# Performance work log

Hardware: AMD Instinct MI355X
Metric: run time of the kernel (lower is better)

## Reference

```python
import jax, jax.numpy as jnp
import numpy as np

D = 768          # embedding_dim
H = 8            # attention heads
DH = D // H
HID = 512        # hidden_dim
N_LAYERS = 3     # graph conv layers
N_ETYPES = 5
LN_EPS = 1e-5


def setup_inputs() -> dict:
    key = jax.random.key(0)
    ks = jax.random.split(key, 32)
    N, E = 4096, 131072
    s = lambda fan: 1.0 / np.sqrt(fan)
    inp = {
        'node_features': jax.random.normal(ks[0], (N, D), jnp.float32),
        'edge_indices': jax.random.randint(ks[1], (2, E), 0, N, jnp.int64),
        'edge_types': jax.random.randint(ks[2], (E,), 0, N_ETYPES, jnp.int64),
        'node_types': jax.random.randint(ks[3], (N,), 0, 3, jnp.int64),
        # embedding tables
        'statute_emb': jax.random.normal(ks[4], (1000, D), jnp.float32),
        'case_emb': jax.random.normal(ks[5], (5000, D), jnp.float32),
        'article_emb': jax.random.normal(ks[6], (2000, D), jnp.float32),
        # per-layer conv params (stacked over 3 layers)
        'conv_msg_W': jax.random.uniform(ks[7], (N_LAYERS, N_ETYPES, D, D), jnp.float32, -s(D), s(D)),
        'conv_msg_b': jax.random.uniform(ks[8], (N_LAYERS, N_ETYPES, D), jnp.float32, -s(D), s(D)),
        'conv_upd_W': jax.random.uniform(ks[9], (N_LAYERS, D, 2 * D), jnp.float32, -s(2 * D), s(2 * D)),
        'conv_upd_b': jax.random.uniform(ks[10], (N_LAYERS, D), jnp.float32, -s(2 * D), s(2 * D)),
        'conv_ln_g': jnp.ones((N_LAYERS, D), jnp.float32),
        'conv_ln_b': jnp.zeros((N_LAYERS, D), jnp.float32),
        # MultiheadAttention params
        'in_proj_W': jax.random.uniform(ks[11], (3 * D, D), jnp.float32, -s(D), s(D)),
        'in_proj_b': jnp.zeros((3 * D,), jnp.float32),
        'out_proj_W': jax.random.uniform(ks[12], (D, D), jnp.float32, -s(D), s(D)),
        'out_proj_b': jnp.zeros((D,), jnp.float32),
        # network analyzer MLP
        'an_W1': jax.random.uniform(ks[13], (HID, D), jnp.float32, -s(D), s(D)),
        'an_b1': jax.random.uniform(ks[14], (HID,), jnp.float32, -s(D), s(D)),
        'an_W2': jax.random.uniform(ks[15], (HID // 2, HID), jnp.float32, -s(HID), s(HID)),
        'an_b2': jax.random.uniform(ks[16], (HID // 2,), jnp.float32, -s(HID), s(HID)),
        'an_W3': jax.random.uniform(ks[17], (1, HID // 2), jnp.float32, -s(HID // 2), s(HID // 2)),
        'an_b3': jax.random.uniform(ks[18], (1,), jnp.float32, -s(HID // 2), s(HID // 2)),
    }
    return inp


def _layer_norm(h, g, b):
    mu = h.mean(-1, keepdims=True)
    var = ((h - mu) ** 2).mean(-1, keepdims=True)
    return g * (h - mu) / jnp.sqrt(var + LN_EPS) + b


def _conv_layer(x, msg_W, msg_b, upd_W, upd_b, ln_g, ln_b, src, tgt, etypes):
    # x: [N, D]; src/tgt: [E]; etypes: [E]
    src_feats = x[src]                               # gather [E, D]
    agg = jnp.zeros_like(x)
    for t in range(N_ETYPES):                        # small fixed loop over edge types
        mask = (etypes == t)[:, None]
        msgs = jnp.where(mask, src_feats @ msg_W[t].T + msg_b[t], 0.0)
        agg = agg + jax.ops.segment_sum(msgs, tgt, num_segments=x.shape[0])
    combined = jnp.concatenate([x, agg], axis=-1)    # [N, 2D]
    upd = jax.nn.relu(combined @ upd_W.T + upd_b)    # dropout is identity in eval
    return _layer_norm(x + upd, ln_g, ln_b)


def reference(node_features, edge_indices, edge_types, node_types,
              statute_emb, case_emb, article_emb,
              conv_msg_W, conv_msg_b, conv_upd_W, conv_upd_b, conv_ln_g, conv_ln_b,
              in_proj_W, in_proj_b, out_proj_W, out_proj_b,
              an_W1, an_b1, an_W2, an_b2, an_W3, an_b3):
    N = node_features.shape[0]
    idx = jnp.arange(N)
    # per-node-type embedding lookup (i % table_size), vectorized
    emb = jnp.where((node_types == 0)[:, None], statute_emb[idx % 1000],
          jnp.where((node_types == 1)[:, None], case_emb[idx % 5000],
                    article_emb[idx % 2000]))
    x = node_features + emb

    src, tgt = edge_indices[0], edge_indices[1]
    for l in range(N_LAYERS):
        x = _conv_layer(x, conv_msg_W[l], conv_msg_b[l], conv_upd_W[l], conv_upd_b[l],
                        conv_ln_g[l], conv_ln_b[l], src, tgt, edge_types)

    # self-attention over all nodes (batch of 1), torch MHA semantics, eval mode
    qkv = x @ in_proj_W.T + in_proj_b                # [N, 3D]
    q, k, v = jnp.split(qkv, 3, axis=-1)
    to_h = lambda t: t.reshape(N, H, DH).transpose(1, 0, 2)   # [H, N, DH]
    q, k, v = to_h(q), to_h(k), to_h(v)
    scores = jnp.einsum('hqd,hkd->hqk', q, k) / jnp.sqrt(jnp.float32(DH))
    attn = jax.nn.softmax(scores, axis=-1)           # [H, N, N]
    ctx = jnp.einsum('hqk,hkd->hqd', attn, v).transpose(1, 0, 2).reshape(N, D)
    graph_repr = ctx @ out_proj_W.T + out_proj_b     # [N, D]
    attn_weights = attn.mean(0)                      # averaged over heads [N, N]

    pooled = graph_repr.mean(axis=0)                 # [D]
    h = jax.nn.relu(pooled @ an_W1.T + an_b1)
    h = jax.nn.relu(h @ an_W2.T + an_b2)
    network_score = jax.nn.sigmoid(h @ an_W3.T + an_b3)

    return x, graph_repr, network_score, attn_weights
```

## Files before the change

### kernel.cpp

```cpp
#include <hip/hip_runtime.h>

typedef unsigned short u16;
typedef unsigned int u32;
typedef __attribute__((ext_vector_type(4))) float f32x4;
typedef __attribute__((ext_vector_type(8))) __bf16 bf16x8;
typedef __attribute__((ext_vector_type(4))) unsigned int u32x4;
typedef __attribute__((ext_vector_type(2))) unsigned int u32x2;

#define DEV static __device__ __forceinline__

#define NNODE 4096
#define DMODEL 768
#define NEDGE 131072

static constexpr size_t OFF_X     = 0;
static constexpr size_t OFF_X2    = 12582912;
static constexpr size_t OFF_AMSG  = 25165824;
static constexpr size_t OFF_AUPD  = 31457280;
static constexpr size_t OFF_WMSG  = 44040192;
static constexpr size_t OFF_WUPD  = 61734912;
static constexpr size_t OFF_WIP   = 68812800;
static constexpr size_t OFF_WOP   = 72351744;
static constexpr size_t OFF_Q     = 73531392;
static constexpr size_t OFF_K     = 79822848;
static constexpr size_t OFF_V     = 86114304;
static constexpr size_t OFF_CTX   = 92405760;
static constexpr size_t OFF_STATS = 98697216;
static constexpr size_t OFF_ML    = 98959360;
static constexpr size_t OFF_DEG   = 100007936;
static constexpr size_t OFF_OFFS  = 100024320;
static constexpr size_t OFF_CUR   = 100040960;
static constexpr size_t OFF_PACK  = 100057344;
static constexpr size_t OFF_PART  = 100581632;
static constexpr size_t OFF_POOL  = 101368064;
static constexpr size_t OFF_H1    = 101371136;
static constexpr size_t OFF_H2    = 101373184;
static constexpr size_t OFF_Y     = 101374208;
static constexpr size_t WS_TOTAL  = 132831488;

__device__ __attribute__((aligned(256))) unsigned char g_ws[WS_TOTAL];

DEV u16 f2bf(float f) {
  return __builtin_bit_cast(u16, (__bf16)f);
}
DEV float bf2f(u16 h) {
  union { unsigned u; float f; } v; v.u = ((unsigned)h) << 16;
  return v.f;
}
DEV void gl_lds16(const void* g, void* l) {
  __builtin_amdgcn_global_load_lds((const __attribute__((address_space(1))) void*)g,
                                   (__attribute__((address_space(3))) void*)l, 16, 0, 0);
}
DEV f32x4 mfma16(bf16x8 a, bf16x8 b, f32x4 c) {
  return __builtin_amdgcn_mfma_f32_16x16x32_bf16(a, b, c, 0, 0, 0);
}
DEV void xcd_swz(int& z, int& bmy, int& bnx) {
  const int gx = gridDim.x, gy = gridDim.y;
  const int nwg = gx * gy * gridDim.z;
  const int L = blockIdx.x + gx * (blockIdx.y + gy * blockIdx.z);
  const int R = (L & 7) * (nwg >> 3) + (L >> 3);
  const int gxy = gx * gy;
  z = R / gxy;
  const int rem = R - z * gxy;
  bmy = rem / gx;
  bnx = rem - bmy * gx;
}

__global__ void zero_kernel(int* p, int n) {
  int i = blockIdx.x * 256 + threadIdx.x;
  if (i < n) p[i] = 0;
}
__global__ void deg_kernel(const int* __restrict__ ei, int* __restrict__ deg) {
  int e = blockIdx.x * 256 + threadIdx.x;
  atomicAdd(&deg[ei[NEDGE + e]], 1);
}
__global__ void scan_kernel(const int* __restrict__ deg, int* __restrict__ offs, int* __restrict__ cur) {
  __shared__ int buf[1024];
  int t = threadIdx.x;
  int v0 = deg[t*4], v1 = deg[t*4+1], v2 = deg[t*4+2], v3 = deg[t*4+3];
  int s = v0 + v1 + v2 + v3;
  buf[t] = s;
  __syncthreads();
  for (int off = 1; off < 1024; off <<= 1) {
    int add = (t >= off) ? buf[t - off] : 0;
    __syncthreads();
    buf[t] += add;
    __syncthreads();
  }
  int run = buf[t] - s;
  offs[t*4] = run; cur[t*4] = run; run += v0;
  offs[t*4+1] = run; cur[t*4+1] = run; run += v1;
  offs[t*4+2] = run; cur[t*4+2] = run; run += v2;
  offs[t*4+3] = run; cur[t*4+3] = run; run += v3;
  if (t == 1023) offs[4096] = run;
}
__global__ void scatter_kernel(const int* __restrict__ ei, const int* __restrict__ ety,
                               int* __restrict__ cur, int* __restrict__ pack) {
  int e = blockIdx.x * 256 + threadIdx.x;
  int tg = ei[NEDGE + e];
  int pos = atomicAdd(&cur[tg], 1);
  pack[pos] = ei[e] | (ety[e] << 12);
}

__global__ void convert_bf_kernel(const float* __restrict__ W, u16* __restrict__ out, int total4) {
  for (int i = blockIdx.x * 256 + threadIdx.x; i < total4; i += gridDim.x * 256) {
    f32x4 w = *(const f32x4*)(W + (size_t)i * 4);
    u32x2 o;
    o.x = (u32)f2bf(w.x) | ((u32)f2bf(w.y) << 16);
    o.y = (u32)f2bf(w.z) | ((u32)f2bf(w.w) << 16);
    *(u32x2*)(out + (size_t)i * 4) = o;
  }
}

__global__ void embed_kernel(const float* __restrict__ nf, const int* __restrict__ nty,
                             const float* __restrict__ se, const float* __restrict__ ce,
                             const float* __restrict__ ae,
                             float* __restrict__ x, u16* __restrict__ Amsg, u16* __restrict__ Aupd) {
  int v = blockIdx.x, t = threadIdx.x;
  int typ = nty[v];
  const float* tab = (typ == 0) ? se + (size_t)(v % 1000) * 768
                   : (typ == 1) ? ce + (size_t)(v % 5000) * 768
                                : ae + (size_t)(v % 2000) * 768;
  #pragma unroll
  for (int i = 0; i < 3; ++i) {
    int c = t + i * 256;
    float f = nf[(size_t)v * 768 + c] + tab[c];
    x[(size_t)v * 768 + c] = f;
    u16 hi = f2bf(f);
    Amsg[(size_t)v * 768 + c] = hi;
    Aupd[(size_t)v * 1536 + c] = hi;
  }
}

template<int EPI>
__global__ void __launch_bounds__(256, 3)
gemm_bt(const u16* __restrict__ A, int lda,
        const u16* __restrict__ B0, int ldb, int K,
        const float* __restrict__ bias0,
        float* __restrict__ C0, int ldc,
        const float* __restrict__ resid,
        u16* __restrict__ oq, u16* __restrict__ okk, u16* __restrict__ ov,
        long zsB, int zsBias, long zsC)
{
  __shared__ alignas(16) u16 sA[8192];
  __shared__ alignas(16) u16 sB[8192];
  const int tid = threadIdx.x;
  const int lane = tid & 63, wid = tid >> 6;
  const int wr = wid >> 1, wc = wid & 1;
  const int li = lane & 15, g = lane >> 4;
  int z, bmy, bnx;
  xcd_swz(z, bmy, bnx);
  const int bm = bmy * 128, bn = bnx * 128;
  const u16* B = B0 + (size_t)z * zsB;
  const float* bias = bias0 + (size_t)z * zsBias;

  const int srow = tid >> 3;
  const int scol = ((tid & 7) ^ (srow & 7)) * 8;
  const u16* Ag = A + (size_t)(bm + srow) * lda + scol;
  const u16* Bg = B + (size_t)(bn + srow) * ldb + scol;
  char* sAw = (char*)sA + wid * 1024;
  char* sBw = (char*)sB + wid * 1024;

  f32x4 acc[4][4];
  const f32x4 vz = {0.f, 0.f, 0.f, 0.f};
  #pragma unroll
  for (int i = 0; i < 4; ++i)
    #pragma unroll
    for (int j = 0; j < 4; ++j) acc[i][j] = vz;

  for (int k0 = 0; k0 < K; k0 += 64) {
    __syncthreads();
    #pragma unroll
    for (int is = 0; is < 4; ++is) {
      gl_lds16(Ag + (size_t)is * 32 * lda + k0, sAw + is * 4096);
      gl_lds16(Bg + (size_t)is * 32 * ldb + k0, sBw + is * 4096);
    }
    __syncthreads();
    #pragma unroll
    for (int kc = 0; kc < 2; ++kc) {
      bf16x8 av[4], bv[4];
      #pragma unroll
      for (int mt = 0; mt < 4; ++mt) {
        int row = wr * 64 + mt * 16 + li;
        av[mt] = *(const bf16x8*)((const char*)sA + row * 128 + ((kc * 64 + g * 16) ^ ((row & 7) << 4)));
      }
      #pragma unroll
      for (int nt = 0; nt < 4; ++nt) {
        int row = wc * 64 + nt * 16 + li;
        bv[nt] = *(const bf16x8*)((const char*)sB + row * 128 + ((kc * 64 + g * 16) ^ ((row & 7) << 4)));
      }
      #pragma unroll
      for (int mt = 0; mt < 4; ++mt)
        #pragma unroll
        for (int nt = 0; nt < 4; ++nt)
          acc[mt][nt] = mfma16(av[mt], bv[nt], acc[mt][nt]);
    }
  }
  #pragma unroll
  for (int mt = 0; mt < 4; ++mt) {
    #pragma unroll
    for (int nt = 0; nt < 4; ++nt) {
      #pragma unroll
      for (int r = 0; r < 4; ++r) {
        int gr = bm + wr * 64 + mt * 16 + g * 4 + r;
        int gc = bn + wc * 64 + nt * 16 + li;
        float v = acc[mt][nt][r] + bias[gc];
        if (EPI == 0) {
          C0[(size_t)z * zsC + (size_t)gr * ldc + gc] = v;
        } else if (EPI == 1) {
          C0[(size_t)gr * ldc + gc] = fmaxf(v, 0.f) + resid[(size_t)gr * 768 + gc];
        } else if (EPI == 3) {
          oq[(size_t)z * zsC + (size_t)gr * ldc + gc] = f2bf(v);
        } else {
          int part = gc / 768;
          int j = gc - part * 768;
          int h = j / 96, d = j - h * 96;
          if (part == 0)      oq[((size_t)(h << 12) + gr) * 96 + d] = f2bf(v * 0.10206207261596575f);
          else if (part == 1) okk[((size_t)(h << 12) + gr) * 96 + d] = f2bf(v);
          else                ov[((size_t)h * 96 + d) * 4096 + gr] = f2bf(v);
        }
      }
    }
  }
}

template<int EPI>
__global__ void __launch_bounds__(256, 3)
gemm_bt64(const u16* __restrict__ A, int lda,
          const u16* __restrict__ B0, int ldb, int K,
          const float* __restrict__ bias,
          float* __restrict__ C0, int ldc,
          const float* __restrict__ resid)
{
  __shared__ alignas(16) u16 sA[8192];
  __shared__ alignas(16) u16 sB[4096];
  const int tid = threadIdx.x;
  const int lane = tid & 63, wid = tid >> 6;
  const int wr = wid >> 1, wc = wid & 1;
  const int li = lane & 15, g = lane >> 4;
  int z, bmy, bnx;
  xcd_swz(z, bmy, bnx);
  const int bm = bmy * 128, bn = bnx * 64;

  const int srow = tid >> 3;
  const int scol = ((tid & 7) ^ (srow & 7)) * 8;
  const u16* Ag = A + (size_t)(bm + srow) * lda + scol;
  const u16* Bg = B0 + (size_t)(bn + srow) * ldb + scol;
  char* sAw = (char*)sA + wid * 1024;
  char* sBw = (char*)sB + wid * 1024;

  f32x4 acc[4][2];
  const f32x4 vz = {0.f, 0.f, 0.f, 0.f};
  #pragma unroll
  for (int i = 0; i < 4; ++i) { acc[i][0] = vz; acc[i][1] = vz; }

  for (int k0 = 0; k0 < K; k0 += 64) {
    __syncthreads();
    #pragma unroll
    for (int is = 0; is < 4; ++is)
      gl_lds16(Ag + (size_t)is * 32 * lda + k0, sAw + is * 4096);
    #pragma unroll
    for (int is = 0; is < 2; ++is)
      gl_lds16(Bg + (size_t)is * 32 * ldb + k0, sBw + is * 4096);
    __syncthreads();
    #pragma unroll
    for (int kc = 0; kc < 2; ++kc) {
      bf16x8 av[4], bv[2];
      #pragma unroll
      for (int mt = 0; mt < 4; ++mt) {
        int row = wr * 64 + mt * 16 + li;
        av[mt] = *(const bf16x8*)((const char*)sA + row * 128 + ((kc * 64 + g * 16) ^ ((row & 7) << 4)));
      }
      #pragma unroll
      for (int nt = 0; nt < 2; ++nt) {
        int row = wc * 32 + nt * 16 + li;
        bv[nt] = *(const bf16x8*)((const char*)sB + row * 128 + ((kc * 64 + g * 16) ^ ((row & 7) << 4)));
      }
      #pragma unroll
      for (int mt = 0; mt < 4; ++mt)
        #pragma unroll
        for (int nt = 0; nt < 2; ++nt)
          acc[mt][nt] = mfma16(av[mt], bv[nt], acc[mt][nt]);
    }
  }
  #pragma unroll
  for (int mt = 0; mt < 4; ++mt) {
    #pragma unroll
    for (int nt = 0; nt < 2; ++nt) {
      #pragma unroll
      for (int r = 0; r < 4; ++r) {
        int gr = bm + wr * 64 + mt * 16 + g * 4 + r;
        int gc = bn + wc * 32 + nt * 16 + li;
        float v = acc[mt][nt][r] + bias[gc];
        if (EPI == 0) C0[(size_t)gr * ldc + gc] = v;
        else          C0[(size_t)gr * ldc + gc] = fmaxf(v, 0.f) + resid[(size_t)gr * 768 + gc];
      }
    }
  }
}

__global__ void agg_kernel(const u16* __restrict__ Y, const int* __restrict__ offs,
                           const int* __restrict__ pack, u16* __restrict__ Aupd) {
  const int v = blockIdx.x, t = threadIdx.x;
  float a0 = 0.f, a1 = 0.f, a2 = 0.f, a3 = 0.f;
  const int beg = offs[v], end = offs[v + 1];
  const u32* Yw = (const u32*)Y;
  for (int i = beg; i < end; ++i) {
    int p = pack[i];
    u32x2 w = *(const u32x2*)(Yw + (size_t)p * 384 + t * 2);
    a0 += bf2f((u16)(w.x & 0xffffu));
    a1 += bf2f((u16)(w.x >> 16));
    a2 += bf2f((u16)(w.y & 0xffffu));
    a3 += bf2f((u16)(w.y >> 16));
  }
  u32x2 o;
  o.x = (u32)f2bf(a0) | ((u32)f2bf(a1) << 16);
  o.y = (u32)f2bf(a2) | ((u32)f2bf(a3) << 16);
  *(u32x2*)((u32*)(Aupd + (size_t)v * 1536 + 768) + t * 2) = o;
}

__global__ void ln_kernel(const float* __restrict__ xin, const float* __restrict__ gam,
                          const float* __restrict__ bet,
                          float* __restrict__ x, u16* __restrict__ Amsg, u16* __restrict__ Aupd,
                          float* __restrict__ xcopy) {
  __shared__ float red[256];
  int v = blockIdx.x, t = threadIdx.x;
  const float* r = xin + (size_t)v * 768;
  float v0 = r[t], v1 = r[t + 256], v2 = r[t + 512];
  red[t] = v0 + v1 + v2;
  __syncthreads();
  for (int off = 128; off > 0; off >>= 1) { if (t < off) red[t] += red[t + off]; __syncthreads(); }
  float mu = red[0] * (1.f / 768.f);
  __syncthreads();
  float d0 = v0 - mu, d1 = v1 - mu, d2 = v2 - mu;
  red[t] = d0 * d0 + d1 * d1 + d2 * d2;
  __syncthreads();
  for (int off = 128; off > 0; off >>= 1) { if (t < off) red[t] += red[t + off]; __syncthreads(); }
  float rstd = rsqrtf(red[0] * (1.f / 768.f) + 1e-5f);
  float dv[3] = {d0, d1, d2};
  #pragma unroll
  for (int i = 0; i < 3; ++i) {
    int c = t + i * 256;
    float y = gam[c] * dv[i] * rstd + bet[c];
    x[(size_t)v * 768 + c] = y;
    if (xcopy) xcopy[(size_t)v * 768 + c] = y;
    u16 hi = f2bf(y);
    Amsg[(size_t)v * 768 + c] = hi;
    Aupd[(size_t)v * 1536 + c] = hi;
  }
}

__global__ void __launch_bounds__(256, 3)
flash_kernel(const u16* __restrict__ Qb, const u16* __restrict__ Kb,
             const u16* __restrict__ Vtb, u16* __restrict__ Opb,
             float* __restrict__ Mp, float* __restrict__ Lp) {
  __shared__ alignas(16) u16 sK[6144];
  __shared__ alignas(16) u16 sV[6144];
  __shared__ alignas(16) u16 sP[4][2048];
  const int tid = threadIdx.x, lane = tid & 63, wid = tid >> 6;
  const int li = lane & 15, g = lane >> 4;
  const int R = blockIdx.x + 32 * (blockIdx.y + 8 * blockIdx.z);
  const int L = (R & 7) * 128 + (R >> 3);
  const int qt = L & 31, h = (L >> 5) & 7, kcb = L >> 8;
  const int vrow = tid >> 3, vcol = (tid & 7) ^ (vrow & 7);

  const u16* Qg = Qb + ((size_t)(h << 12) + qt * 128 + wid * 32 + li) * 96 + g * 8;
  bf16x8 aq0[3], aq1[3];
  #pragma unroll
  for (int kc = 0; kc < 3; ++kc) {
    aq0[kc] = *(const bf16x8*)(Qg + kc * 32);
    aq1[kc] = *(const bf16x8*)(Qg + 1536 + kc * 32);
  }

  float m0 = -1e30f, l0 = 0.f, m1 = -1e30f, l1 = 0.f;
  const f32x4 vz = {0.f, 0.f, 0.f, 0.f};
  f32x4 o0[6], o1[6];
  #pragma unroll
  for (int dt = 0; dt < 6; ++dt) { o0[dt] = vz; o1[dt] = vz; }

  const char* Kg = (const char*)(Kb + (size_t)(h << 12) * 96);
  const char* Vg = (const char*)(Vtb + (size_t)h * 96 * 4096);
  char* sKb = (char*)sK; char* sVb = (char*)sV; char* sPb = (char*)sP[wid];

  for (int kt = kcb * 16; kt < kcb * 16 + 16; ++kt) {
    __syncthreads();
    #pragma unroll
    for (int j = 0; j < 3; ++j) {
      gl_lds16(Kg + ((size_t)(kt * 64 + lane) * 96 + j * 32 + wid * 8) * 2, sKb + j * 4096 + wid * 1024);
      gl_lds16(Vg + (size_t)(j * 32 + vrow) * 8192 + kt * 128 + vcol * 16, sVb + j * 4096 + wid * 1024);
    }
    __syncthreads();

    f32x4 s0[4], s1[4];
    __builtin_amdgcn_s_setprio(1);
    #pragma unroll
    for (int nt = 0; nt < 4; ++nt) {
      s0[nt] = vz; s1[nt] = vz;
      #pragma unroll
      for (int kc = 0; kc < 3; ++kc) {
        bf16x8 bk = *(const bf16x8*)(sKb + kc * 4096 + g * 1024 + (nt * 16 + li) * 16);
        s0[nt] = mfma16(bk, aq0[kc], s0[nt]);
        s1[nt] = mfma16(bk, aq1[kc], s1[nt]);
      }
    }
    __builtin_amdgcn_s_setprio(0);

    {
      float mx = fmaxf(fmaxf(fmaxf(s0[0][0], s0[0][1]), fmaxf(s0[0][2], s0[0][3])),
                       fmaxf(fmaxf(s0[1][0], s0[1][1]), fmaxf(s0[1][2], s0[1][3])));
      mx = fmaxf(mx, fmaxf(fmaxf(fmaxf(s0[2][0], s0[2][1]), fmaxf(s0[2][2], s0[2][3])),
                           fmaxf(fmaxf(s0[3][0], s0[3][1]), fmaxf(s0[3][2], s0[3][3]))));
      mx = fmaxf(mx, __shfl_xor(mx, 16));
      mx = fmaxf(mx, __shfl_xor(mx, 32));
      float mnew = fmaxf(m0, mx);
      float alpha = __expf(m0 - mnew);
      float rs = 0.f;
      #pragma unroll
      for (int nt = 0; nt < 4; ++nt)
        #pragma unroll
        for (int r = 0; r < 4; ++r) { float p = __expf(s0[nt][r] - mnew); s0[nt][r] = p; rs += p; }
      rs += __shfl_xor(rs, 16);
      rs += __shfl_xor(rs, 32);
      l0 = l0 * alpha + rs;
      m0 = mnew;
      #pragma unroll
      for (int dt = 0; dt < 6; ++dt) o0[dt] *= alpha;
      #pragma unroll
      for (int nt = 0; nt < 4; ++nt)
        #pragma unroll
        for (int r0 = 0; r0 < 4; r0 += 2) {
          u32 w = (u32)f2bf(s0[nt][r0]) | ((u32)f2bf(s0[nt][r0 + 1]) << 16);
          *(u32*)(sPb + li * 128 + (((nt * 16 + g * 4 + r0) * 2) ^ ((li & 7) << 4))) = w;
        }
    }
    {
      float mx = fmaxf(fmaxf(fmaxf(s1[0][0], s1[0][1]), fmaxf(s1[0][2], s1[0][3])),
                       fmaxf(fmaxf(s1[1][0], s1[1][1]), fmaxf(s1[1][2], s1[1][3])));
      mx = fmaxf(mx, fmaxf(fmaxf(fmaxf(s1[2][0], s1[2][1]), fmaxf(s1[2][2], s1[2][3])),
                           fmaxf(fmaxf(s1[3][0], s1[3][1]), fmaxf(s1[3][2], s1[3][3]))));
      mx = fmaxf(mx, __shfl_xor(mx, 16));
      mx = fmaxf(mx, __shfl_xor(mx, 32));
      float mnew = fmaxf(m1, mx);
      float alpha = __expf(m1 - mnew);
      float rs = 0.f;
      #pragma unroll
      for (int nt = 0; nt < 4; ++nt)
        #pragma unroll
        for (int r = 0; r < 4; ++r) { float p = __expf(s1[nt][r] - mnew); s1[nt][r] = p; rs += p; }
      rs += __shfl_xor(rs, 16);
      rs += __shfl_xor(rs, 32);
      l1 = l1 * alpha + rs;
      m1 = mnew;
      #pragma unroll
      for (int dt = 0; dt < 6; ++dt) o1[dt] *= alpha;
      #pragma unroll
      for (int nt = 0; nt < 4; ++nt)
        #pragma unroll
        for (int r0 = 0; r0 < 4; r0 += 2) {
          u32 w = (u32)f2bf(s1[nt][r0]) | ((u32)f2bf(s1[nt][r0 + 1]) << 16);
          *(u32*)(sPb + (16 + li) * 128 + (((nt * 16 + g * 4 + r0) * 2) ^ ((li & 7) << 4))) = w;
        }
    }

    __builtin_amdgcn_s_setprio(1);
    #pragma unroll
    for (int kc2 = 0; kc2 < 2; ++kc2) {
      bf16x8 pa0 = *(const bf16x8*)(sPb + li * 128 + ((kc2 * 64 + g * 16) ^ ((li & 7) << 4)));
      bf16x8 pa1 = *(const bf16x8*)(sPb + (16 + li) * 128 + ((kc2 * 64 + g * 16) ^ ((li & 7) << 4)));
      #pragma unroll
      for (int dt = 0; dt < 6; ++dt) {
        int d = dt * 16 + li;
        bf16x8 bvv = *(const bf16x8*)(sVb + d * 128 + ((kc2 * 64 + g * 16) ^ ((d & 7) << 4)));
        o0[dt] = mfma16(pa0, bvv, o0[dt]);
        o1[dt] = mfma16(pa1, bvv, o1[dt]);
      }
    }
    __builtin_amdgcn_s_setprio(0);
  }
  int bq = qt * 128 + wid * 32;
  size_t cb = (size_t)(((kcb * 8 + h) << 12));
  #pragma unroll
  for (int dt = 0; dt < 6; ++dt)
    #pragma unroll
    for (int r = 0; r < 4; ++r) {
      int d = dt * 16 + li;
      Opb[(cb + bq + g * 4 + r) * 96 + d] = f2bf(o0[dt][r]);
      Opb[(cb + bq + 16 + g * 4 + r) * 96 + d] = f2bf(o1[dt][r]);
    }
  if (g == 0) {
    Mp[cb + bq + li] = m0;      Lp[cb + bq + li] = l0;
    Mp[cb + bq + 16 + li] = m1; Lp[cb + bq + 16 + li] = l1;
  }
}

__global__ void merge_kernel(const u16* __restrict__ Opb, const float* __restrict__ Mp,
                             const float* __restrict__ Lp,
                             u16* __restrict__ ctxb, float* __restrict__ stats) {
  int row = blockIdx.x, t = threadIdx.x;
  #pragma unroll
  for (int i = 0; i < 3; ++i) {
    int idx = t + i * 256;
    int h = idx / 96, d = idx - h * 96;
    int base = (h << 12) + row;
    float m0 = Mp[base], m1 = Mp[32768 + base], m2 = Mp[65536 + base], m3 = Mp[98304 + base];
    float M = fmaxf(fmaxf(m0, m1), fmaxf(m2, m3));
    float w0 = __expf(m0 - M), w1 = __expf(m1 - M), w2 = __expf(m2 - M), w3 = __expf(m3 - M);
    float L = w0 * Lp[base] + w1 * Lp[32768 + base] + w2 * Lp[65536 + base] + w3 * Lp[98304 + base];
    float o = w0 * bf2f(Opb[(size_t)base * 96 + d])
            + w1 * bf2f(Opb[(size_t)(32768 + base) * 96 + d])
            + w2 * bf2f(Opb[(size_t)(65536 + base) * 96 + d])
            + w3 * bf2f(Opb[(size_t)(98304 + base) * 96 + d]);
    float invl = 1.f / L;
    ctxb[(size_t)row * 768 + idx] = f2bf(o * invl);
    if (d == 0) {
      stats[base] = M;
      stats[32768 + base] = invl;
    }
  }
}

__global__ void __launch_bounds__(256, 3)
mean_kernel(const u16* __restrict__ Qb, const u16* __restrict__ Kb,
            const float* __restrict__ stats, float* __restrict__ out) {
  __shared__ alignas(16) u16 sQ[12288];
  __shared__ alignas(16) u16 sK2[6144];
  const int tid = threadIdx.x, lane = tid & 63, wid = tid >> 6;
  const int li = lane & 15, g = lane >> 4;
  const int q0 = blockIdx.x * 128, k0 = blockIdx.y * 64;
  const f32x4 vz = {0.f, 0.f, 0.f, 0.f};
  f32x4 macc0[4], macc1[4];
  #pragma unroll
  for (int nt = 0; nt < 4; ++nt) { macc0[nt] = vz; macc1[nt] = vz; }
  char* sQb = (char*)sQ; char* sKb = (char*)sK2;
  const int rq = (wid & 1) * 64 + lane;
  const int ccb = wid >> 1;

  for (int h = 0; h < 8; ++h) {
    __syncthreads();
    #pragma unroll
    for (int i = 0; i < 6; ++i) {
      int cc = i * 2 + ccb, kc = cc >> 2, gg = cc & 3;
      gl_lds16((const char*)Qb + ((size_t)(h << 12) + q0 + rq) * 192 + kc * 64 + gg * 16,
               sQb + kc * 8192 + gg * 2048 + (wid & 1) * 1024);
    }
    #pragma unroll
    for (int i = 0; i < 3; ++i) {
      int c = i * 4 + wid, kc = c >> 2, gg = c & 3;
      gl_lds16((const char*)Kb + ((size_t)(h << 12) + k0 + lane) * 192 + kc * 64 + gg * 16,
               sKb + kc * 4096 + gg * 1024);
    }
    __syncthreads();

    bf16x8 a20[3], a21[3];
    #pragma unroll
    for (int kc = 0; kc < 3; ++kc) {
      a20[kc] = *(const bf16x8*)(sQb + kc * 8192 + g * 2048 + (wid * 32 + li) * 16);
      a21[kc] = *(const bf16x8*)(sQb + kc * 8192 + g * 2048 + (wid * 32 + 16 + li) * 16);
    }
    f32x4 s0[4], s1[4];
    __builtin_amdgcn_s_setprio(1);
    #pragma unroll
    for (int nt = 0; nt < 4; ++nt) {
      s0[nt] = vz; s1[nt] = vz;
      #pragma unroll
      for (int kc = 0; kc < 3; ++kc) {
        bf16x8 bk = *(const bf16x8*)(sKb + kc * 4096 + g * 1024 + (nt * 16 + li) * 16);
        s0[nt] = mfma16(a20[kc], bk, s0[nt]);
        s1[nt] = mfma16(a21[kc], bk, s1[nt]);
      }
    }
    __builtin_amdgcn_s_setprio(0);
    #pragma unroll
    for (int r = 0; r < 4; ++r) {
      int row0 = q0 + wid * 32 + g * 4 + r;
      float mm0 = stats[(h << 12) + row0];
      float si0 = 0.125f * stats[32768 + (h << 12) + row0];
      int row1 = row0 + 16;
      float mm1 = stats[(h << 12) + row1];
      float si1 = 0.125f * stats[32768 + (h << 12) + row1];
      #pragma unroll
      for (int nt = 0; nt < 4; ++nt) {
        macc0[nt][r] += __expf(s0[nt][r] - mm0) * si0;
        macc1[nt][r] += __expf(s1[nt][r] - mm1) * si1;
      }
    }
  }
  #pragma unroll
  for (int nt = 0; nt < 4; ++nt)
    #pragma unroll
    for (int r = 0; r < 4; ++r) {
      out[(size_t)(q0 + wid * 32 + g * 4 + r) * 4096 + k0 + nt * 16 + li] = macc0[nt][r];
      out[(size_t)(q0 + wid * 32 + 16 + g * 4 + r) * 4096 + k0 + nt * 16 + li] = macc1[nt][r];
    }
}

__global__ void colsum_kernel(const float* __restrict__ gr, float* __restrict__ part) {
  int b = blockIdx.x, t = threadIdx.x;
  float s0 = 0.f, s1 = 0.f, s2 = 0.f;
  for (int rr = 0; rr < 16; ++rr) {
    const float* row = gr + (size_t)(b * 16 + rr) * 768;
    s0 += row[t]; s1 += row[t + 256]; s2 += row[t + 512];
  }
  part[b * 768 + t] = s0; part[b * 768 + t + 256] = s1; part[b * 768 + t + 512] = s2;
}
__global__ void pool_kernel(const float* __restrict__ part, float* __restrict__ pool) {
  int t = blockIdx.x * 256 + threadIdx.x;
  float s = 0.f;
  for (int b = 0; b < 256; ++b) s += part[b * 768 + t];
  pool[t] = s * (1.f / 4096.f);
}
template<int KDIM>
__global__ void mlp_fc_kernel(const float* __restrict__ in, const float* __restrict__ Wm,
                              const float* __restrict__ bb, float* __restrict__ outv) {
  int o = blockIdx.x * 4 + (threadIdx.x >> 6);
  int lane = threadIdx.x & 63;
  const float* w = Wm + (size_t)o * KDIM;
  float s = 0.f;
  #pragma unroll
  for (int k = lane; k < KDIM; k += 64) s += w[k] * in[k];
  s += __shfl_xor(s, 1);  s += __shfl_xor(s, 2);  s += __shfl_xor(s, 4);
  s += __shfl_xor(s, 8);  s += __shfl_xor(s, 16); s += __shfl_xor(s, 32);
  if (lane == 0) outv[o] = fmaxf(s + bb[o], 0.f);
}
__global__ void mlp3_kernel(const float* __restrict__ h2,
                            const float* __restrict__ W3, const float* __restrict__ b3,
                            float* __restrict__ out) {
  __shared__ float red[256];
  int t = threadIdx.x;
  red[t] = W3[t] * h2[t];
  __syncthreads();
  for (int off = 128; off > 0; off >>= 1) { if (t < off) red[t] += red[t + off]; __syncthreads(); }
  if (t == 0) out[0] = 1.f / (1.f + __expf(-(red[0] + b3[0])));
}

extern "C" void kernel_launch(void* const* d_in, const int* in_sizes, int n_in,
                              void* d_out, int out_size, void* d_ws, size_t ws_size,
                              hipStream_t stream) {
  const float* nf   = (const float*)d_in[0];
  const int*   ei   = (const int*)d_in[1];
  const int*   ety  = (const int*)d_in[2];
  const int*   nty  = (const int*)d_in[3];
  const float* se   = (const float*)d_in[4];
  const float* ce   = (const float*)d_in[5];
  const float* ae   = (const float*)d_in[6];
  const float* msgW = (const float*)d_in[7];
  const float* msgb = (const float*)d_in[8];
  const float* updW = (const float*)d_in[9];
  const float* updb = (const float*)d_in[10];
  const float* lng  = (const float*)d_in[11];
  const float* lnb  = (const float*)d_in[12];
  const float* ipW  = (const float*)d_in[13];
  const float* ipb  = (const float*)d_in[14];
  const float* opW  = (const float*)d_in[15];
  const float* opb  = (const float*)d_in[16];
  const float* aW1  = (const float*)d_in[17];
  const float* ab1  = (const float*)d_in[18];
  const float* aW2  = (const float*)d_in[19];
  const float* ab2  = (const float*)d_in[20];
  const float* aW3  = (const float*)d_in[21];
  const float* ab3  = (const float*)d_in[22];

  void* wsp = nullptr;
  hipGetSymbolAddress(&wsp, HIP_SYMBOL(g_ws));
  unsigned char* W = (unsigned char*)wsp;

  float* x     = (float*)(W + OFF_X);
  float* x2    = (float*)(W + OFF_X2);
  u16* Amsg    = (u16*)(W + OFF_AMSG);
  u16* Aupd    = (u16*)(W + OFF_AUPD);
  u16* Wmsg    = (u16*)(W + OFF_WMSG);
  u16* Wupd    = (u16*)(W + OFF_WUPD);
  u16* Wip     = (u16*)(W + OFF_WIP);
  u16* Wop     = (u16*)(W + OFF_WOP);
  u16* Qb      = (u16*)(W + OFF_Q);
  u16* Kb      = (u16*)(W + OFF_K);
  u16* Vtb     = (u16*)(W + OFF_V);
  u16* Ctxb    = (u16*)(W + OFF_CTX);
  float* stats = (float*)(W + OFF_STATS);
  float* Mp    = (float*)(W + OFF_ML);
  float* Lp    = Mp + 131072;
  int* deg     = (int*)(W + OFF_DEG);
  int* offs    = (int*)(W + OFF_OFFS);
  int* cur     = (int*)(W + OFF_CUR);
  int* pack    = (int*)(W + OFF_PACK);
  float* part  = (float*)(W + OFF_PART);
  float* pool  = (float*)(W + OFF_POOL);
  float* h1b   = (float*)(W + OFF_H1);
  float* h2b   = (float*)(W + OFF_H2);
  u16*   Yb    = (u16*)(W + OFF_Y);

  float* out_x    = (float*)d_out;
  float* out_gr   = out_x + (size_t)NNODE * DMODEL;
  float* out_sc   = out_gr + (size_t)NNODE * DMODEL;
  float* out_attn = out_sc + 1;
  u16*   Opb      = (u16*)out_attn;

  zero_kernel<<<16, 256, 0, stream>>>(deg, NNODE);
  deg_kernel<<<NEDGE / 256, 256, 0, stream>>>(ei, deg);
  scan_kernel<<<1, 1024, 0, stream>>>(deg, offs, cur);
  scatter_kernel<<<NEDGE / 256, 256, 0, stream>>>(ei, ety, cur, pack);

  convert_bf_kernel<<<2048, 256, 0, stream>>>(msgW, Wmsg, 3 * 5 * 768 * 768 / 4);
  convert_bf_kernel<<<1024, 256, 0, stream>>>(updW, Wupd, 3 * 768 * 1536 / 4);
  convert_bf_kernel<<<1024, 256, 0, stream>>>(ipW, Wip, 2304 * 768 / 4);
  convert_bf_kernel<<<512, 256, 0, stream>>>(opW, Wop, 768 * 768 / 4);

  embed_kernel<<<NNODE, 256, 0, stream>>>(nf, nty, se, ce, ae, x, Amsg, Aupd);

  for (int l = 0; l < 3; ++l) {
    gemm_bt<3><<<dim3(6, 32, 5), 256, 0, stream>>>(Amsg, 768,
        Wmsg + (size_t)l * 5 * 768 * 768, 768, 768,
        msgb + (size_t)l * 5 * 768, nullptr, 768, nullptr, Yb, nullptr, nullptr,
        (long)768 * 768, 768, (long)NNODE * DMODEL);
    agg_kernel<<<NNODE, 192, 0, stream>>>(Yb, offs, pack, Aupd);
    gemm_bt64<1><<<dim3(12, 32), 256, 0, stream>>>(Aupd, 1536,
        Wupd + (size_t)l * 768 * 1536, 1536, 1536,
        updb + (size_t)l * 768, x2, 768, x);
    ln_kernel<<<NNODE, 256, 0, stream>>>(x2, lng + (size_t)l * 768, lnb + (size_t)l * 768,
        x, Amsg, Aupd, (l == 2) ? out_x : nullptr);
  }

  gemm_bt<2><<<dim3(18, 32, 1), 256, 0, stream>>>(Amsg, 768, Wip, 768, 768,
      ipb, nullptr, 0, nullptr, Qb, Kb, Vtb, 0, 0, 0);
  flash_kernel<<<dim3(32, 8, 4), 256, 0, stream>>>(Qb, Kb, Vtb, Opb, Mp, Lp);
  merge_kernel<<<NNODE, 256, 0, stream>>>(Opb, Mp, Lp, Ctxb, stats);
  mean_kernel<<<dim3(32, 64), 256, 0, stream>>>(Qb, Kb, stats, out_attn);
  gemm_bt64<0><<<dim3(12, 32), 256, 0, stream>>>(Ctxb, 768, Wop, 768, 768,
      opb, out_gr, 768, nullptr);

  colsum_kernel<<<256, 256, 0, stream>>>(out_gr, part);
  pool_kernel<<<3, 256, 0, stream>>>(part, pool);
  mlp_fc_kernel<768><<<128, 256, 0, stream>>>(pool, aW1, ab1, h1b);
  mlp_fc_kernel<512><<<64, 256, 0, stream>>>(h1b, aW2, ab2, h2b);
  mlp3_kernel<<<1, 256, 0, stream>>>(h2b, aW3, ab3, out_sc);
}
```

Before: 607.2 us.

## Use 128x64 GEMM for QKV projection, widen P stores, remap mean-kernel blocks

The QKV input projection moves from the 128x128-tile gemm_bt to the 128x64-tile gemm_bt64, with the head-split epilogue carried over, so the grid grows from 576 to 1152 blocks for better occupancy across CUs. In the flash kernel the bf16 probability tile is written to LDS as 8-byte stores instead of pairs of 4-byte stores. The mean_kernel now remaps block indices so that consecutive blocks, which are likely spread across XCDs, share tiles and get better L2 locality. The smaller GEMM tile reloads the A operand more often.

Measured after the change: 616.3 us. No clear change (+1.5%).

```diff
diff --git a/kernel.cpp b/kernel.cpp
--- a/kernel.cpp
+++ b/kernel.cpp
@@ -211,13 +211,6 @@
           C0[(size_t)gr * ldc + gc] = fmaxf(v, 0.f) + resid[(size_t)gr * 768 + gc];
         } else if (EPI == 3) {
           oq[(size_t)z * zsC + (size_t)gr * ldc + gc] = f2bf(v);
-        } else {
-          int part = gc / 768;
-          int j = gc - part * 768;
-          int h = j / 96, d = j - h * 96;
-          if (part == 0)      oq[((size_t)(h << 12) + gr) * 96 + d] = f2bf(v * 0.10206207261596575f);
-          else if (part == 1) okk[((size_t)(h << 12) + gr) * 96 + d] = f2bf(v);
-          else                ov[((size_t)h * 96 + d) * 4096 + gr] = f2bf(v);
         }
       }
     }
@@ -230,7 +223,8 @@
           const u16* __restrict__ B0, int ldb, int K,
           const float* __restrict__ bias,
           float* __restrict__ C0, int ldc,
-          const float* __restrict__ resid)
+          const float* __restrict__ resid,
+          u16* __restrict__ oq, u16* __restrict__ okk, u16* __restrict__ ov)
 {
   __shared__ alignas(16) u16 sA[8192];
   __shared__ alignas(16) u16 sB[4096];
@@ -292,8 +286,18 @@
         int gr = bm + wr * 64 + mt * 16 + g * 4 + r;
         int gc = bn + wc * 32 + nt * 16 + li;
         float v = acc[mt][nt][r] + bias[gc];
-        if (EPI == 0) C0[(size_t)gr * ldc + gc] = v;
-        else          C0[(size_t)gr * ldc + gc] = fmaxf(v, 0.f) + resid[(size_t)gr * 768 + gc];
+        if (EPI == 0) {
+          C0[(size_t)gr * ldc + gc] = v;
+        } else if (EPI == 1) {
+          C0[(size_t)gr * ldc + gc] = fmaxf(v, 0.f) + resid[(size_t)gr * 768 + gc];
+        } else {
+          int part = gc / 768;
+          int j = gc - part * 768;
+          int h = j / 96, d = j - h * 96;
+          if (part == 0)      oq[((size_t)(h << 12) + gr) * 96 + d] = f2bf(v * 0.10206207261596575f);
+          else if (part == 1) okk[((size_t)(h << 12) + gr) * 96 + d] = f2bf(v);
+          else                ov[((size_t)h * 96 + d) * 4096 + gr] = f2bf(v);
+        }
       }
     }
   }
@@ -426,12 +430,12 @@
       #pragma unroll
       for (int dt = 0; dt < 6; ++dt) o0[dt] *= alpha;
       #pragma unroll
-      for (int nt = 0; nt < 4; ++nt)
-        #pragma unroll
-        for (int r0 = 0; r0 < 4; r0 += 2) {
-          u32 w = (u32)f2bf(s0[nt][r0]) | ((u32)f2bf(s0[nt][r0 + 1]) << 16);
-          *(u32*)(sPb + li * 128 + (((nt * 16 + g * 4 + r0) * 2) ^ ((li & 7) << 4))) = w;
-        }
+      for (int nt = 0; nt < 4; ++nt) {
+        u32x2 w;
+        w.x = (u32)f2bf(s0[nt][0]) | ((u32)f2bf(s0[nt][1]) << 16);
+        w.y = (u32)f2bf(s0[nt][2]) | ((u32)f2bf(s0[nt][3]) << 16);
+        *(u32x2*)(sPb + li * 128 + (((nt * 16 + g * 4) * 2) ^ ((li & 7) << 4))) = w;
+      }
     }
     {
       float mx = fmaxf(fmaxf(fmaxf(s1[0][0], s1[0][1]), fmaxf(s1[0][2], s1[0][3])),
@@ -454,12 +458,12 @@
       #pragma unroll
       for (int dt = 0; dt < 6; ++dt) o1[dt] *= alpha;
       #pragma unroll
-      for (int nt = 0; nt < 4; ++nt)
-        #pragma unroll
-        for (int r0 = 0; r0 < 4; r0 += 2) {
-          u32 w = (u32)f2bf(s1[nt][r0]) | ((u32)f2bf(s1[nt][r0 + 1]) << 16);
-          *(u32*)(sPb + (16 + li) * 128 + (((nt * 16 + g * 4 + r0) * 2) ^ ((li & 7) << 4))) = w;
-        }
+      for (int nt = 0; nt < 4; ++nt) {
+        u32x2 w;
+        w.x = (u32)f2bf(s1[nt][0]) | ((u32)f2bf(s1[nt][1]) << 16);
+        w.y = (u32)f2bf(s1[nt][2]) | ((u32)f2bf(s1[nt][3]) << 16);
+        *(u32x2*)(sPb + (16 + li) * 128 + (((nt * 16 + g * 4) * 2) ^ ((li & 7) << 4))) = w;
+      }
     }
 
     __builtin_amdgcn_s_setprio(1);
@@ -526,7 +530,9 @@
   __shared__ alignas(16) u16 sK2[6144];
   const int tid = threadIdx.x, lane = tid & 63, wid = tid >> 6;
   const int li = lane & 15, g = lane >> 4;
-  const int q0 = blockIdx.x * 128, k0 = blockIdx.y * 64;
+  const int R = blockIdx.x + 32 * blockIdx.y;
+  const int L = (R & 7) * 256 + (R >> 3);
+  const int q0 = (L & 31) * 128, k0 = (L >> 5) * 64;
   const f32x4 vz = {0.f, 0.f, 0.f, 0.f};
   f32x4 macc0[4], macc1[4];
   #pragma unroll
@@ -715,18 +721,18 @@
     agg_kernel<<<NNODE, 192, 0, stream>>>(Yb, offs, pack, Aupd);
     gemm_bt64<1><<<dim3(12, 32), 256, 0, stream>>>(Aupd, 1536,
         Wupd + (size_t)l * 768 * 1536, 1536, 1536,
-        updb + (size_t)l * 768, x2, 768, x);
+        updb + (size_t)l * 768, x2, 768, x, nullptr, nullptr, nullptr);
     ln_kernel<<<NNODE, 256, 0, stream>>>(x2, lng + (size_t)l * 768, lnb + (size_t)l * 768,
         x, Amsg, Aupd, (l == 2) ? out_x : nullptr);
   }
 
-  gemm_bt<2><<<dim3(18, 32, 1), 256, 0, stream>>>(Amsg, 768, Wip, 768, 768,
-      ipb, nullptr, 0, nullptr, Qb, Kb, Vtb, 0, 0, 0);
+  gemm_bt64<2><<<dim3(36, 32), 256, 0, stream>>>(Amsg, 768, Wip, 768, 768,
+      ipb, nullptr, 0, nullptr, Qb, Kb, Vtb);
   flash_kernel<<<dim3(32, 8, 4), 256, 0, stream>>>(Qb, Kb, Vtb, Opb, Mp, Lp);
   merge_kernel<<<NNODE, 256, 0, stream>>>(Opb, Mp, Lp, Ctxb, stats);
   mean_kernel<<<dim3(32, 64), 256, 0, stream>>>(Qb, Kb, stats, out_attn);
   gemm_bt64<0><<<dim3(12, 32), 256, 0, stream>>>(Ctxb, 768, Wop, 768, 768,
-      opb, out_gr, 768, nullptr);
+      opb, out_gr, 768, nullptr, nullptr, nullptr, nullptr);
 
   colsum_kernel<<<256, 256, 0, stream>>>(out_gr, part);
   pool_kernel<<<3, 256, 0, stream>>>(part, pool);
```
